# Optimization experiments

Hardware: AMD Instinct MI355X
Metric: run time of the kernel (lower is better)

The kernel has to match this reference:

```python
import jax, jax.numpy as jnp
import numpy as np

N = 100000   # nodes
E = 1600000  # edges (avg degree 16)
F_IN = 50    # dataset.num_features
C = 32       # dataset.num_classes == hidden == out channels


def setup_inputs() -> dict:
    key = jax.random.key(0)
    ks = jax.random.split(key, 12)
    x = jax.random.normal(ks[0], (N, F_IN), dtype=jnp.float32)
    edge_index = jax.random.randint(ks[1], (2, E), 0, N, dtype=jnp.int64)
    dims = [(F_IN, C), (C, C), (C, C)]
    inp = {"x": x, "edge_index": edge_index}
    for i, (din, dout) in enumerate(dims, start=1):
        s = 1.0 / np.sqrt(din)
        inp[f"Wl{i}"] = jax.random.uniform(ks[2 + 3 * (i - 1)], (din, dout), jnp.float32, -s, s)
        inp[f"bl{i}"] = jax.random.uniform(ks[3 + 3 * (i - 1)], (dout,), jnp.float32, -s, s)
        inp[f"Wr{i}"] = jax.random.uniform(ks[4 + 3 * (i - 1)], (din, dout), jnp.float32, -s, s)
    return inp


def _sage_conv(x, src, dst, Wl, bl, Wr):
    # message = x[src]; scatter-max into dst; lin_l(agg) + lin_r(x)
    msg = x[src]                                      # [E, d_in]
    agg = jax.ops.segment_max(msg, dst, num_segments=N)
    agg = jnp.where(jnp.isfinite(agg), agg, jnp.zeros((), agg.dtype))  # empty segments -> 0
    return agg @ Wl + bl + x @ Wr


def reference(x, edge_index, Wl1, bl1, Wr1, Wl2, bl2, Wr2, Wl3, bl3, Wr3):
    src, dst = edge_index[0], edge_index[1]
    h = jax.nn.relu(_sage_conv(x, src, dst, Wl1, bl1, Wr1))
    h = jax.nn.relu(_sage_conv(h, src, dst, Wl2, bl2, Wr2))
    h = _sage_conv(h, src, dst, Wl3, bl3, Wr3)
    return jax.nn.log_softmax(h, axis=1)
```

## Files before the change

kernel.cpp:

```cpp
#include <hip/hip_runtime.h>
#include <math.h>

#define NN 100000
#define CD 32
#define NPB 4

#define B1N ((NN + 255) >> 8)
#define EPB_A 2048

typedef unsigned int   uint32;
typedef unsigned short ushort16;

__device__ __forceinline__ ushort16 f2b(float f) {
    uint32 u = __float_as_uint(f);
    u = (u + 0x7FFFu + ((u >> 16) & 1u)) >> 16;
    return (ushort16)u;
}
__device__ __forceinline__ float b2f_lo(uint32 u) { return __uint_as_float(u << 16); }
__device__ __forceinline__ float b2f_hi(uint32 u) { return __uint_as_float(u & 0xFFFF0000u); }

__device__ __forceinline__ int edge_is64(const void* edge) {
    const long long* p = (const long long*)edge;
    int lane = threadIdx.x & 63;
    int bad = 0;
    for (int i = lane; i < 512; i += 64) {
        long long v = p[i];
        if (v < 0 || v >= NN) bad = 1;
    }
    unsigned long long anybad = __ballot(bad);
    return (anybad == 0ULL) ? 1 : 0;
}

__device__ __forceinline__ int load_idx(const void* edge, int i, int is64) {
    if (is64) return (int)((const long long*)edge)[i];
    return ((const int*)edge)[i];
}

__global__ void cvt_x_kernel(const float* __restrict__ x, uint32* __restrict__ xb) {
    const int t = blockIdx.x * blockDim.x + threadIdx.x;
    if (t >= NN * 32) return;
    const int n = t >> 5;
    const int c = t & 31;
    if (c >= 25) { xb[t] = 0; return; }
    float2 v = *(const float2*)&x[n * 50 + 2 * c];
    xb[t] = (uint32)f2b(v.x) | ((uint32)f2b(v.y) << 16);
}


__global__ __launch_bounds__(256) void hist_kernel(const void* edge, int E,
                                                   int* __restrict__ hist) {
    __shared__ int lh[B1N];
    const int is64 = edge_is64(edge);
    const int t = threadIdx.x;
    for (int b = t; b < B1N; b += 256) lh[b] = 0;
    __syncthreads();
    const int e0 = blockIdx.x * EPB_A + t;
#pragma unroll
    for (int k = 0; k < 8; ++k) {
        int e = e0 + k * 256;
        if (e < E) {
            int d = load_idx(edge, E + e, is64);
            atomicAdd(&lh[d >> 8], 1);
        }
    }
    __syncthreads();
    int* gh = hist + (size_t)blockIdx.x * B1N;
    for (int b = t; b < B1N; b += 256) gh[b] = lh[b];
}

__global__ __launch_bounds__(256) void scanA_kernel(int* __restrict__ hist,
                                                    int nblk,
                                                    int* __restrict__ binTotal) {
    __shared__ int ts[256];
    const int bin = blockIdx.x;
    const int t = threadIdx.x;
    const int base = t * 4;
    int v0 = (base + 0 < nblk) ? hist[(size_t)(base + 0) * B1N + bin] : 0;
    int v1 = (base + 1 < nblk) ? hist[(size_t)(base + 1) * B1N + bin] : 0;
    int v2 = (base + 2 < nblk) ? hist[(size_t)(base + 2) * B1N + bin] : 0;
    int v3 = (base + 3 < nblk) ? hist[(size_t)(base + 3) * B1N + bin] : 0;
    const int s = v0 + v1 + v2 + v3;
    ts[t] = s;
    __syncthreads();
    for (int off = 1; off < 256; off <<= 1) {
        int u = (t >= off) ? ts[t - off] : 0;
        __syncthreads();
        ts[t] += u;
        __syncthreads();
    }
    int e = ts[t] - s;
    if (base + 0 < nblk) { hist[(size_t)(base + 0) * B1N + bin] = e; e += v0; }
    if (base + 1 < nblk) { hist[(size_t)(base + 1) * B1N + bin] = e; e += v1; }
    if (base + 2 < nblk) { hist[(size_t)(base + 2) * B1N + bin] = e; e += v2; }
    if (base + 3 < nblk) { hist[(size_t)(base + 3) * B1N + bin] = e; e += v3; }
    if (t == 255) binTotal[bin] = ts[255];
}

__device__ __forceinline__ void scan_bins_lds(const int* __restrict__ binTotal,
                                              int* ts, int* lbase) {
    const int t = threadIdx.x;
    const int base = t * 2;
    const int v0 = (base + 0 < B1N) ? binTotal[base + 0] : 0;
    const int v1 = (base + 1 < B1N) ? binTotal[base + 1] : 0;
    const int s = v0 + v1;
    ts[t] = s;
    __syncthreads();
    for (int off = 1; off < 256; off <<= 1) {
        int u = (t >= off) ? ts[t - off] : 0;
        __syncthreads();
        ts[t] += u;
        __syncthreads();
    }
    const int e = ts[t] - s;
    if (base + 0 < B1N) lbase[base + 0] = e;
    if (base + 1 < B1N) lbase[base + 1] = e + v0;
    if (t == 255) lbase[B1N] = ts[255];
    __syncthreads();
}

__global__ __launch_bounds__(256) void scatter_kernel(const void* edge, int E,
                                                      const int* __restrict__ hist,
                                                      const int* __restrict__ binTotal,
                                                      uint32* __restrict__ bucketed) {
    __shared__ int ts[256];
    __shared__ int lbase[B1N + 1];
    __shared__ int cur[B1N];
    const int is64 = edge_is64(edge);
    const int t = threadIdx.x;
    scan_bins_lds(binTotal, ts, lbase);
    const int* gh = hist + (size_t)blockIdx.x * B1N;
    for (int b = t; b < B1N; b += 256) cur[b] = lbase[b] + gh[b];
    __syncthreads();
    const int e0 = blockIdx.x * EPB_A + t;
#pragma unroll
    for (int k = 0; k < 8; ++k) {
        int e = e0 + k * 256;
        if (e < E) {
            int s = load_idx(edge, e, is64);
            int d = load_idx(edge, E + e, is64);
            int pos = atomicAdd(&cur[d >> 8], 1);
            bucketed[pos] = (uint32)s | ((uint32)(d & 255) << 17);
        }
    }
}

__global__ __launch_bounds__(256) void bucket_kernel(const uint32* __restrict__ bucketed,
                                                     const int* __restrict__ binTotal,
                                                     int* __restrict__ offsets,
                                                     int* __restrict__ csr_src) {
    __shared__ int ts[256];
    __shared__ int lbase[B1N + 1];
    __shared__ int h[256];
    __shared__ int sc[256];
    __shared__ int cur[256];
    const int bkt = blockIdx.x;
    const int t = threadIdx.x;
    scan_bins_lds(binTotal, ts, lbase);
    const int start = lbase[bkt];
    const int end   = lbase[bkt + 1];
    h[t] = 0;
    __syncthreads();
    for (int i = start + t; i < end; i += 256)
        atomicAdd(&h[bucketed[i] >> 17], 1);
    __syncthreads();
    const int v = h[t];
    sc[t] = v;
    __syncthreads();
    for (int off = 1; off < 256; off <<= 1) {
        int u = (t >= off) ? sc[t - off] : 0;
        __syncthreads();
        sc[t] += u;
        __syncthreads();
    }
    const int excl = sc[t] - v;
    const int node = bkt * 256 + t;
    if (node < NN) offsets[node] = start + excl;
    cur[t] = start + excl;
    __syncthreads();
    for (int i = start + t; i < end; i += 256) {
        uint32 p = bucketed[i];
        int pos = atomicAdd(&cur[p >> 17], 1);
        csr_src[pos] = (int)(p & 0x1FFFFu);
    }
    if (bkt == B1N - 1 && t == 0) offsets[NN] = end;
}


__global__ void gather50_kernel(const uint32* __restrict__ hb,
                                const int* __restrict__ offsets,
                                const int* __restrict__ csr_src,
                                uint32* __restrict__ aggB) {
    const int tid  = threadIdx.x;
    const int g    = tid >> 6;
    const int lane = tid & 63;
    const int p    = lane >> 5;
    const int j    = lane & 31;
    const int n    = blockIdx.x * NPB + g;
    if (n >= NN) return;

    const float NEG = -INFINITY;
    const int beg = offsets[n];
    const int end = offsets[n + 1];
    const char* hbase = (const char*)hb;
    const uint32 joff = (uint32)(j << 2);
    const int lb = p << 5;

    float lo_[8], hi_[8];
#pragma unroll
    for (int k = 0; k < 8; ++k) { lo_[k] = NEG; hi_[k] = NEG; }

    for (int ib = beg; ib < end; ib += 64) {
        const int rem = end - ib;
        const int mm  = rem < 64 ? rem : 64;
        const int myidx = 2 * j + p;
        int sidx = 0;
        if (myidx < mm) sidx = csr_src[ib + myidx];
        int k = p;
        for (; k + 14 < mm; k += 16) {
            const int kh = lb + (k >> 1);
#pragma unroll
            for (int kk = 0; kk < 8; ++kk) {
                int s = __shfl(sidx, kh + kk);
                uint32 u = *(const uint32*)(hbase + ((((uint32)s) << 7) | joff));
                lo_[kk] = fmaxf(lo_[kk], b2f_lo(u));
                hi_[kk] = fmaxf(hi_[kk], b2f_hi(u));
            }
        }
        for (; k + 6 < mm; k += 8) {
            const int kh = lb + (k >> 1);
#pragma unroll
            for (int kk = 0; kk < 4; ++kk) {
                int s = __shfl(sidx, kh + kk);
                uint32 u = *(const uint32*)(hbase + ((((uint32)s) << 7) | joff));
                lo_[kk] = fmaxf(lo_[kk], b2f_lo(u));
                hi_[kk] = fmaxf(hi_[kk], b2f_hi(u));
            }
        }
        for (; k < mm; k += 2) {
            int s = __shfl(sidx, lb + (k >> 1));
            uint32 u = *(const uint32*)(hbase + ((((uint32)s) << 7) | joff));
            lo_[0] = fmaxf(lo_[0], b2f_lo(u));
            hi_[0] = fmaxf(hi_[0], b2f_hi(u));
        }
    }
#pragma unroll
    for (int off2 = 4; off2 > 0; off2 >>= 1)
#pragma unroll
        for (int k = 0; k < off2; ++k) {
            lo_[k] = fmaxf(lo_[k], lo_[k + off2]);
            hi_[k] = fmaxf(hi_[k], hi_[k + off2]);
        }
    float lo = lo_[0], hi = hi_[0];
    lo = fmaxf(lo, __shfl_xor(lo, 32));
    hi = fmaxf(hi, __shfl_xor(hi, 32));
    lo = (lo == NEG) ? 0.0f : lo;
    hi = (hi == NEG) ? 0.0f : hi;
    if (p == 0 && j < 25) {
        aggB[(size_t)n * 32 + j] =
            (__float_as_uint(lo) >> 16) | (__float_as_uint(hi) & 0xFFFF0000u);
    }
}

__global__ void gather32_kernel(const uint32* __restrict__ hb,
                                const int* __restrict__ offsets,
                                const int* __restrict__ csr_src,
                                uint32* __restrict__ aggB) {
    const int tid  = threadIdx.x;
    const int g    = tid >> 6;
    const int lane = tid & 63;
    const int e    = lane >> 4;
    const int c    = lane & 15;
    const int n    = blockIdx.x * NPB + g;
    if (n >= NN) return;

    const float NEG = -INFINITY;
    const int beg = offsets[n];
    const int end = offsets[n + 1];
    const char* hbase = (const char*)hb;
    const uint32 coff = (uint32)(c << 2);
    const int lb = e << 4;

    float l0 = NEG, h0 = NEG, l1 = NEG, h1 = NEG;
    float l2 = NEG, h2 = NEG, l3 = NEG, h3 = NEG;

    for (int ib = beg; ib < end; ib += 64) {
        const int rem = end - ib;
        const int mm  = rem < 64 ? rem : 64;
        const int myidx = 4 * c + e;
        int sidx = 0;
        if (myidx < mm) sidx = csr_src[ib + myidx];
        int k = e;
        for (; k + 12 < mm; k += 16) {
            const int m = lb + (k >> 2);
            int s0 = __shfl(sidx, m);
            int s1 = __shfl(sidx, m + 1);
            int s2 = __shfl(sidx, m + 2);
            int s3 = __shfl(sidx, m + 3);
            uint32 u0 = *(const uint32*)(hbase + ((((uint32)s0) << 6) | coff));
            uint32 u1 = *(const uint32*)(hbase + ((((uint32)s1) << 6) | coff));
            uint32 u2 = *(const uint32*)(hbase + ((((uint32)s2) << 6) | coff));
            uint32 u3 = *(const uint32*)(hbase + ((((uint32)s3) << 6) | coff));
            l0 = fmaxf(l0, b2f_lo(u0)); h0 = fmaxf(h0, b2f_hi(u0));
            l1 = fmaxf(l1, b2f_lo(u1)); h1 = fmaxf(h1, b2f_hi(u1));
            l2 = fmaxf(l2, b2f_lo(u2)); h2 = fmaxf(h2, b2f_hi(u2));
            l3 = fmaxf(l3, b2f_lo(u3)); h3 = fmaxf(h3, b2f_hi(u3));
        }
        for (; k < mm; k += 4) {
            int s = __shfl(sidx, lb + (k >> 2));
            uint32 u = *(const uint32*)(hbase + ((((uint32)s) << 6) | coff));
            l0 = fmaxf(l0, b2f_lo(u)); h0 = fmaxf(h0, b2f_hi(u));
        }
    }
    float lo = fmaxf(fmaxf(l0, l1), fmaxf(l2, l3));
    float hi = fmaxf(fmaxf(h0, h1), fmaxf(h2, h3));
    lo = fmaxf(lo, __shfl_xor(lo, 16));
    hi = fmaxf(hi, __shfl_xor(hi, 16));
    lo = fmaxf(lo, __shfl_xor(lo, 32));
    hi = fmaxf(hi, __shfl_xor(hi, 32));
    lo = (lo == NEG) ? 0.0f : lo;
    hi = (hi == NEG) ? 0.0f : hi;
    if (lane < 16) {
        aggB[(size_t)n * 16 + lane] =
            (__float_as_uint(lo) >> 16) | (__float_as_uint(hi) & 0xFFFF0000u);
    }
}

template <int DIN, int ASTR, int HSTR, int OSTR, int MODE>
__global__ void dense_kernel(const uint32* __restrict__ aggB,
                             const uint32* __restrict__ hB,
                             const float* __restrict__ Wl,
                             const float* __restrict__ bl,
                             const float* __restrict__ Wr,
                             void* __restrict__ out_v) {
    const int n = blockIdx.x * blockDim.x + threadIdx.x;
    if (n >= NN) return;

    float acc[CD];
#pragma unroll
    for (int j = 0; j < CD; ++j) acc[j] = bl[j];

    {
        const uint32* row = aggB + (size_t)n * ASTR;
        for (int c = 0; c < DIN / 4; ++c) {
            uint2 u = *(const uint2*)&row[c * 2];
            float d0 = b2f_lo(u.x), d1 = b2f_hi(u.x);
            float d2 = b2f_lo(u.y), d3 = b2f_hi(u.y);
            const float* w = Wl + c * 4 * CD;
#pragma unroll
            for (int j = 0; j < CD; ++j)
                acc[j] += d0 * w[j] + d1 * w[CD + j] + d2 * w[2 * CD + j] + d3 * w[3 * CD + j];
        }
        if (DIN % 4) {
            uint32 u = row[(DIN / 4) * 2];
            float d0 = b2f_lo(u), d1 = b2f_hi(u);
            const float* w = Wl + (DIN - 2) * CD;
#pragma unroll
            for (int j = 0; j < CD; ++j)
                acc[j] += d0 * w[j] + d1 * w[CD + j];
        }
    }
    {
        const uint32* row = hB + (size_t)n * HSTR;
        for (int c = 0; c < DIN / 4; ++c) {
            uint2 u = *(const uint2*)&row[c * 2];
            float d0 = b2f_lo(u.x), d1 = b2f_hi(u.x);
            float d2 = b2f_lo(u.y), d3 = b2f_hi(u.y);
            const float* w = Wr + c * 4 * CD;
#pragma unroll
            for (int j = 0; j < CD; ++j)
                acc[j] += d0 * w[j] + d1 * w[CD + j] + d2 * w[2 * CD + j] + d3 * w[3 * CD + j];
        }
        if (DIN % 4) {
            uint32 u = row[(DIN / 4) * 2];
            float d0 = b2f_lo(u), d1 = b2f_hi(u);
            const float* w = Wr + (DIN - 2) * CD;
#pragma unroll
            for (int j = 0; j < CD; ++j)
                acc[j] += d0 * w[j] + d1 * w[CD + j];
        }
    }

    if (MODE == 0) {
        uint32* orow = (uint32*)out_v + (size_t)n * OSTR;
#pragma unroll
        for (int c = 0; c < CD / 2; ++c) {
            float a0 = fmaxf(acc[2 * c],     0.0f);
            float a1 = fmaxf(acc[2 * c + 1], 0.0f);
            orow[c] = (uint32)f2b(a0) | ((uint32)f2b(a1) << 16);
        }
    } else {
        float m = acc[0];
#pragma unroll
        for (int j = 1; j < CD; ++j) m = fmaxf(m, acc[j]);
        float s = 0.0f;
#pragma unroll
        for (int j = 0; j < CD; ++j) s += expf(acc[j] - m);
        const float lse = m + logf(s);
        float* orow = (float*)out_v + (size_t)n * CD;
#pragma unroll
        for (int j = 0; j < CD; ++j) orow[j] = acc[j] - lse;
    }
}

extern "C" void kernel_launch(void* const* d_in, const int* in_sizes, int n_in,
                              void* d_out, int out_size, void* d_ws, size_t ws_size,
                              hipStream_t stream) {
    const float* x    = (const float*)d_in[0];
    const void*  edge = d_in[1];
    const float* Wl1 = (const float*)d_in[2];
    const float* bl1 = (const float*)d_in[3];
    const float* Wr1 = (const float*)d_in[4];
    const float* Wl2 = (const float*)d_in[5];
    const float* bl2 = (const float*)d_in[6];
    const float* Wr2 = (const float*)d_in[7];
    const float* Wl3 = (const float*)d_in[8];
    const float* bl3 = (const float*)d_in[9];
    const float* Wr3 = (const float*)d_in[10];

    const int E = in_sizes[1] / 2;

    char* ws = (char*)d_ws;
    size_t off = 0;
    auto carve = [&](size_t bytes) {
        void* p = ws + off;
        off = (off + bytes + 255) & ~(size_t)255;
        return p;
    };
    int*    offsets   = (int*)   carve((size_t)(NN + 1) * 4);
    int*    binTotal  = (int*)   carve((size_t)B1N * 4);
    int*    csr_src   = (int*)   carve((size_t)E * 4);
    uint32* xb        = (uint32*)carve((size_t)NN * 32 * 4);
    uint32* h1b       = (uint32*)carve((size_t)NN * 16 * 4);
    (void)ws_size; (void)n_in; (void)out_size;

    uint32* bucketed = (uint32*)d_out;
    int*    hist     = (int*)((char*)d_out + (((size_t)E * 4 + 255) & ~(size_t)255));
    uint32* agg1 = (uint32*)d_out;
    uint32* agg2 = (uint32*)d_out;
    uint32* h2b  = xb;
    uint32* agg3 = h1b;

    cvt_x_kernel<<<(NN * 32 + 255) / 256, 256, 0, stream>>>(x, xb);

    const int nblkA = (E + EPB_A - 1) / EPB_A;
    hist_kernel<<<nblkA, 256, 0, stream>>>(edge, E, hist);
    scanA_kernel<<<B1N, 256, 0, stream>>>(hist, nblkA, binTotal);
    scatter_kernel<<<nblkA, 256, 0, stream>>>(edge, E, hist, binTotal, bucketed);
    bucket_kernel<<<B1N, 256, 0, stream>>>(bucketed, binTotal, offsets, csr_src);

    const int gb = (NN + NPB - 1) / NPB;
    const int db = (NN + 255) / 256;

    gather50_kernel<<<gb, 256, 0, stream>>>(xb, offsets, csr_src, agg1);
    dense_kernel<50, 32, 32, 16, 0><<<db, 256, 0, stream>>>(agg1, xb, Wl1, bl1, Wr1, h1b);
    gather32_kernel<<<gb, 256, 0, stream>>>(h1b, offsets, csr_src, agg2);
    dense_kernel<32, 16, 16, 16, 0><<<db, 256, 0, stream>>>(agg2, h1b, Wl2, bl2, Wr2, h2b);
    gather32_kernel<<<gb, 256, 0, stream>>>(h2b, offsets, csr_src, agg3);
    dense_kernel<32, 16, 16, 0, 2><<<db, 256, 0, stream>>>(agg3, h2b, Wl3, bl3, Wr3, d_out);
}
```

Baseline: 316.2 us.

## Use order-preserving bf16 keys with packed u16 max, merge cvt into hist kernel

New measurement: 302.7 us. 1.04x faster.

```diff
diff --git a/kernel.cpp b/kernel.cpp
--- a/kernel.cpp
+++ b/kernel.cpp
@@ -18,6 +18,21 @@
 }
 __device__ __forceinline__ float b2f_lo(uint32 u) { return __uint_as_float(u << 16); }
 __device__ __forceinline__ float b2f_hi(uint32 u) { return __uint_as_float(u & 0xFFFF0000u); }
+
+__device__ __forceinline__ uint32 pkmax(uint32 a, uint32 b) {
+    uint32 d;
+    asm("v_pk_max_u16 %0, %1, %2" : "=v"(d) : "v"(a), "v"(b));
+    return d;
+}
+__device__ __forceinline__ uint32 key16(float f) {
+    uint32 b = (uint32)f2b(f);
+    return b ^ ((__float_as_uint(f) >> 31) ? 0xFFFFu : 0x8000u);
+}
+__device__ __forceinline__ uint32 dec_pk(uint32 k) {
+    uint32 m = (~k >> 15) & 0x00010001u;
+    uint32 X = 0x80008000u | ((m << 15) - m);
+    return k ^ X;
+}
 
 __device__ __forceinline__ int edge_is64(const void* edge) {
     const long long* p = (const long long*)edge;
@@ -36,36 +51,38 @@
     return ((const int*)edge)[i];
 }
 
-__global__ void cvt_x_kernel(const float* __restrict__ x, uint32* __restrict__ xb) {
-    const int t = blockIdx.x * blockDim.x + threadIdx.x;
-    if (t >= NN * 32) return;
-    const int n = t >> 5;
-    const int c = t & 31;
-    if (c >= 25) { xb[t] = 0; return; }
-    float2 v = *(const float2*)&x[n * 50 + 2 * c];
-    xb[t] = (uint32)f2b(v.x) | ((uint32)f2b(v.y) << 16);
-}
-
-
-__global__ __launch_bounds__(256) void hist_kernel(const void* edge, int E,
-                                                   int* __restrict__ hist) {
+__global__ __launch_bounds__(256) void cvt_hist_kernel(const float* __restrict__ x,
+                                                       uint32* __restrict__ xb,
+                                                       const void* edge, int E,
+                                                       int* __restrict__ hist,
+                                                       int nblkA) {
     __shared__ int lh[B1N];
-    const int is64 = edge_is64(edge);
     const int t = threadIdx.x;
-    for (int b = t; b < B1N; b += 256) lh[b] = 0;
-    __syncthreads();
-    const int e0 = blockIdx.x * EPB_A + t;
-#pragma unroll
-    for (int k = 0; k < 8; ++k) {
-        int e = e0 + k * 256;
-        if (e < E) {
-            int d = load_idx(edge, E + e, is64);
-            atomicAdd(&lh[d >> 8], 1);
-        }
-    }
-    __syncthreads();
-    int* gh = hist + (size_t)blockIdx.x * B1N;
-    for (int b = t; b < B1N; b += 256) gh[b] = lh[b];
+    if ((int)blockIdx.x < nblkA) {
+        const int is64 = edge_is64(edge);
+        for (int b = t; b < B1N; b += 256) lh[b] = 0;
+        __syncthreads();
+        const int e0 = blockIdx.x * EPB_A + t;
+#pragma unroll
+        for (int k = 0; k < 8; ++k) {
+            int e = e0 + k * 256;
+            if (e < E) {
+                int d = load_idx(edge, E + e, is64);
+                atomicAdd(&lh[d >> 8], 1);
+            }
+        }
+        __syncthreads();
+        int* gh = hist + (size_t)blockIdx.x * B1N;
+        for (int b = t; b < B1N; b += 256) gh[b] = lh[b];
+    } else {
+        const int tt = (blockIdx.x - nblkA) * 256 + t;
+        if (tt >= NN * 32) return;
+        const int n = tt >> 5;
+        const int c = tt & 31;
+        if (c >= 25) { xb[tt] = 0; return; }
+        float2 v = *(const float2*)&x[n * 50 + 2 * c];
+        xb[tt] = key16(v.x) | (key16(v.y) << 16);
+    }
 }
 
 __global__ __launch_bounds__(256) void scanA_kernel(int* __restrict__ hist,
@@ -198,16 +215,15 @@
     const int n    = blockIdx.x * NPB + g;
     if (n >= NN) return;
 
-    const float NEG = -INFINITY;
     const int beg = offsets[n];
     const int end = offsets[n + 1];
     const char* hbase = (const char*)hb;
     const uint32 joff = (uint32)(j << 2);
     const int lb = p << 5;
 
-    float lo_[8], hi_[8];
-#pragma unroll
-    for (int k = 0; k < 8; ++k) { lo_[k] = NEG; hi_[k] = NEG; }
+    uint32 a_[8];
+#pragma unroll
+    for (int k = 0; k < 8; ++k) a_[k] = 0;
 
     for (int ib = beg; ib < end; ib += 64) {
         const int rem = end - ib;
@@ -222,8 +238,7 @@
             for (int kk = 0; kk < 8; ++kk) {
                 int s = __shfl(sidx, kh + kk);
                 uint32 u = *(const uint32*)(hbase + ((((uint32)s) << 7) | joff));
-                lo_[kk] = fmaxf(lo_[kk], b2f_lo(u));
-                hi_[kk] = fmaxf(hi_[kk], b2f_hi(u));
+                a_[kk] = pkmax(a_[kk], u);
             }
         }
         for (; k + 6 < mm; k += 8) {
@@ -232,32 +247,24 @@
             for (int kk = 0; kk < 4; ++kk) {
                 int s = __shfl(sidx, kh + kk);
                 uint32 u = *(const uint32*)(hbase + ((((uint32)s) << 7) | joff));
-                lo_[kk] = fmaxf(lo_[kk], b2f_lo(u));
-                hi_[kk] = fmaxf(hi_[kk], b2f_hi(u));
+                a_[kk] = pkmax(a_[kk], u);
             }
         }
         for (; k < mm; k += 2) {
             int s = __shfl(sidx, lb + (k >> 1));
             uint32 u = *(const uint32*)(hbase + ((((uint32)s) << 7) | joff));
-            lo_[0] = fmaxf(lo_[0], b2f_lo(u));
-            hi_[0] = fmaxf(hi_[0], b2f_hi(u));
+            a_[0] = pkmax(a_[0], u);
         }
     }
 #pragma unroll
     for (int off2 = 4; off2 > 0; off2 >>= 1)
 #pragma unroll
-        for (int k = 0; k < off2; ++k) {
-            lo_[k] = fmaxf(lo_[k], lo_[k + off2]);
-            hi_[k] = fmaxf(hi_[k], hi_[k + off2]);
-        }
-    float lo = lo_[0], hi = hi_[0];
-    lo = fmaxf(lo, __shfl_xor(lo, 32));
-    hi = fmaxf(hi, __shfl_xor(hi, 32));
-    lo = (lo == NEG) ? 0.0f : lo;
-    hi = (hi == NEG) ? 0.0f : hi;
+        for (int k = 0; k < off2; ++k)
+            a_[k] = pkmax(a_[k], a_[k + off2]);
+    uint32 r = a_[0];
+    r = pkmax(r, (uint32)__shfl_xor((int)r, 32));
     if (p == 0 && j < 25) {
-        aggB[(size_t)n * 32 + j] =
-            (__float_as_uint(lo) >> 16) | (__float_as_uint(hi) & 0xFFFF0000u);
+        aggB[(size_t)n * 32 + j] = (beg == end) ? 0x80008000u : r;
     }
 }
 
@@ -273,15 +280,13 @@
     const int n    = blockIdx.x * NPB + g;
     if (n >= NN) return;
 
-    const float NEG = -INFINITY;
     const int beg = offsets[n];
     const int end = offsets[n + 1];
     const char* hbase = (const char*)hb;
     const uint32 coff = (uint32)(c << 2);
     const int lb = e << 4;
 
-    float l0 = NEG, h0 = NEG, l1 = NEG, h1 = NEG;
-    float l2 = NEG, h2 = NEG, l3 = NEG, h3 = NEG;
+    uint32 a0 = 0, a1 = 0, a2 = 0, a3 = 0;
 
     for (int ib = beg; ib < end; ib += 64) {
         const int rem = end - ib;
@@ -300,28 +305,20 @@
             uint32 u1 = *(const uint32*)(hbase + ((((uint32)s1) << 6) | coff));
             uint32 u2 = *(const uint32*)(hbase + ((((uint32)s2) << 6) | coff));
             uint32 u3 = *(const uint32*)(hbase + ((((uint32)s3) << 6) | coff));
-            l0 = fmaxf(l0, b2f_lo(u0)); h0 = fmaxf(h0, b2f_hi(u0));
-            l1 = fmaxf(l1, b2f_lo(u1)); h1 = fmaxf(h1, b2f_hi(u1));
-            l2 = fmaxf(l2, b2f_lo(u2)); h2 = fmaxf(h2, b2f_hi(u2));
-            l3 = fmaxf(l3, b2f_lo(u3)); h3 = fmaxf(h3, b2f_hi(u3));
+            a0 = pkmax(a0, u0); a1 = pkmax(a1, u1);
+            a2 = pkmax(a2, u2); a3 = pkmax(a3, u3);
         }
         for (; k < mm; k += 4) {
             int s = __shfl(sidx, lb + (k >> 2));
             uint32 u = *(const uint32*)(hbase + ((((uint32)s) << 6) | coff));
-            l0 = fmaxf(l0, b2f_lo(u)); h0 = fmaxf(h0, b2f_hi(u));
-        }
-    }
-    float lo = fmaxf(fmaxf(l0, l1), fmaxf(l2, l3));
-    float hi = fmaxf(fmaxf(h0, h1), fmaxf(h2, h3));
-    lo = fmaxf(lo, __shfl_xor(lo, 16));
-    hi = fmaxf(hi, __shfl_xor(hi, 16));
-    lo = fmaxf(lo, __shfl_xor(lo, 32));
-    hi = fmaxf(hi, __shfl_xor(hi, 32));
-    lo = (lo == NEG) ? 0.0f : lo;
-    hi = (hi == NEG) ? 0.0f : hi;
+            a0 = pkmax(a0, u);
+        }
+    }
+    uint32 r = pkmax(pkmax(a0, a1), pkmax(a2, a3));
+    r = pkmax(r, (uint32)__shfl_xor((int)r, 16));
+    r = pkmax(r, (uint32)__shfl_xor((int)r, 32));
     if (lane < 16) {
-        aggB[(size_t)n * 16 + lane] =
-            (__float_as_uint(lo) >> 16) | (__float_as_uint(hi) & 0xFFFF0000u);
+        aggB[(size_t)n * 16 + lane] = (beg == end) ? 0x80008000u : r;
     }
 }
 
@@ -343,6 +340,7 @@
         const uint32* row = aggB + (size_t)n * ASTR;
         for (int c = 0; c < DIN / 4; ++c) {
             uint2 u = *(const uint2*)&row[c * 2];
+            u.x = dec_pk(u.x); u.y = dec_pk(u.y);
             float d0 = b2f_lo(u.x), d1 = b2f_hi(u.x);
             float d2 = b2f_lo(u.y), d3 = b2f_hi(u.y);
             const float* w = Wl + c * 4 * CD;
@@ -351,7 +349,7 @@
                 acc[j] += d0 * w[j] + d1 * w[CD + j] + d2 * w[2 * CD + j] + d3 * w[3 * CD + j];
         }
         if (DIN % 4) {
-            uint32 u = row[(DIN / 4) * 2];
+            uint32 u = dec_pk(row[(DIN / 4) * 2]);
             float d0 = b2f_lo(u), d1 = b2f_hi(u);
             const float* w = Wl + (DIN - 2) * CD;
 #pragma unroll
@@ -363,6 +361,7 @@
         const uint32* row = hB + (size_t)n * HSTR;
         for (int c = 0; c < DIN / 4; ++c) {
             uint2 u = *(const uint2*)&row[c * 2];
+            u.x = dec_pk(u.x); u.y = dec_pk(u.y);
             float d0 = b2f_lo(u.x), d1 = b2f_hi(u.x);
             float d2 = b2f_lo(u.y), d3 = b2f_hi(u.y);
             const float* w = Wr + c * 4 * CD;
@@ -371,7 +370,7 @@
                 acc[j] += d0 * w[j] + d1 * w[CD + j] + d2 * w[2 * CD + j] + d3 * w[3 * CD + j];
         }
         if (DIN % 4) {
-            uint32 u = row[(DIN / 4) * 2];
+            uint32 u = dec_pk(row[(DIN / 4) * 2]);
             float d0 = b2f_lo(u), d1 = b2f_hi(u);
             const float* w = Wr + (DIN - 2) * CD;
 #pragma unroll
@@ -386,7 +385,7 @@
         for (int c = 0; c < CD / 2; ++c) {
             float a0 = fmaxf(acc[2 * c],     0.0f);
             float a1 = fmaxf(acc[2 * c + 1], 0.0f);
-            orow[c] = (uint32)f2b(a0) | ((uint32)f2b(a1) << 16);
+            orow[c] = ((uint32)f2b(a0) | ((uint32)f2b(a1) << 16)) | 0x80008000u;
         }
     } else {
         float m = acc[0];
@@ -440,10 +439,9 @@
     uint32* h2b  = xb;
     uint32* agg3 = h1b;
 
-    cvt_x_kernel<<<(NN * 32 + 255) / 256, 256, 0, stream>>>(x, xb);
-
     const int nblkA = (E + EPB_A - 1) / EPB_A;
-    hist_kernel<<<nblkA, 256, 0, stream>>>(edge, E, hist);
+    const int cvtb  = (NN * 32 + 255) / 256;
+    cvt_hist_kernel<<<nblkA + cvtb, 256, 0, stream>>>(x, xb, edge, E, hist, nblkA);
     scanA_kernel<<<B1N, 256, 0, stream>>>(hist, nblkA, binTotal);
     scatter_kernel<<<nblkA, 256, 0, stream>>>(edge, E, hist, binTotal, bucketed);
     bucket_kernel<<<B1N, 256, 0, stream>>>(bucketed, binTotal, offsets, csr_src);
```
